# Performance work log

Hardware: AMD Instinct MI355X
Metric: run time of the kernel (lower is better)

Reference implementation:

```python
import jax, jax.numpy as jnp
import numpy as np

ROUTING_ROUNDS = 3
EPS = 1e-9

def squash(s, axis):
    # s * ||s||^2 / (1 + ||s||^2) / ||s||
    sn = jnp.sum(s * s, axis=axis, keepdims=True)
    return s * (sn / (1.0 + sn)) * jax.lax.rsqrt(sn + EPS)

def setup_inputs() -> dict:
    key = jax.random.key(0)
    k1, k2 = jax.random.split(key)
    B, N, D = 32, 2048, 32   # batch, input caps num, input caps dim
    C, V = 64, 32            # output caps num, output caps dim
    input_layer = jax.random.normal(k1, (B, N, D), dtype=jnp.float32)
    W = 0.1 * jax.random.normal(k2, (1, N, C, V, D), dtype=jnp.float32)
    return {"input_layer": input_layer, "W": W}

def reference(input_layer, W):
    # input_layer: [B, N, D]; W: [1, N, C, V, D]
    B, N, D = input_layer.shape
    Wn = W[0]  # [N, C, V, D]
    C, V = Wn.shape[1], Wn.shape[2]
    # caps_predicted (u_hat): [B, N, C, V]  (== tf matmul of W_tiled @ caps_output_tiled, squeezed)
    u_hat = jnp.einsum('bnd,ncvd->bncv', input_layer, Wn)
    b = jnp.zeros((B, N, C), dtype=input_layer.dtype)
    v = None
    for _ in range(ROUTING_ROUNDS):
        r = jax.nn.softmax(b, axis=2)                      # [B, N, C]
        s = jnp.einsum('bnc,bncv->bcv', r, u_hat)          # weighted_sum over input caps
        v = squash(s, axis=-1)                             # [B, C, V]
        # agreement = u_hat^T . v : [B, N, C]
        b = b + jnp.einsum('bncv,bcv->bnc', u_hat, v)
    # match original output shape [B, 1, caps_num, vec_len, 1]
    return v[:, None, :, :, None]
```

## Files before the change

kernel.cpp:

```cpp
#include <hip/hip_runtime.h>
#include <hip/hip_bf16.h>


#define B_ 32
#define N_ 2048
#define D_ 32
#define C_ 64
#define V_ 32

typedef __attribute__((ext_vector_type(4))) float f32x4;
typedef __attribute__((ext_vector_type(4))) int i32x4;
typedef __bf16 bf16x8 __attribute__((ext_vector_type(8)));

__device__ __forceinline__ unsigned f2bf1(float f) {
  unsigned u = __builtin_bit_cast(unsigned, f);
  return (u + 0x7FFFu + ((u >> 16) & 1u)) >> 16;
}
__device__ __forceinline__ float bf2f(unsigned h) {
  unsigned u = h << 16;
  return __builtin_bit_cast(float, u);
}

__global__ __launch_bounds__(256) void uhat_kernel(const float* __restrict__ x,
                                                   const float* __restrict__ W,
                                                   unsigned short* __restrict__ uh) {
  const int n = blockIdx.x;
  const int wave = threadIdx.x >> 6;
  const int l = threadIdx.x & 63;
  const int l16 = l & 15, kg = l >> 4;

  __shared__ unsigned short lds[4][32 * 68];
  unsigned short* wlds = lds[wave];

  bf16x8 a[2];
#pragma unroll
  for (int mt = 0; mt < 2; ++mt) {
    const float* xp = x + (((size_t)(mt * 16 + l16)) * N_ + n) * D_ + kg * 8;
    f32x4 x0 = *(const f32x4*)xp;
    f32x4 x1 = *(const f32x4*)(xp + 4);
    i32x4 af;
    af[0] = f2bf1(x0[0]) | (f2bf1(x0[1]) << 16);
    af[1] = f2bf1(x0[2]) | (f2bf1(x0[3]) << 16);
    af[2] = f2bf1(x1[0]) | (f2bf1(x1[1]) << 16);
    af[3] = f2bf1(x1[2]) | (f2bf1(x1[3]) << 16);
    a[mt] = __builtin_bit_cast(bf16x8, af);
  }
  const f32x4 zero = {0.f, 0.f, 0.f, 0.f};
  const int br_f = l >> 1, half = l & 1;

  for (int ph = 0; ph < 8; ++ph) {
#pragma unroll
    for (int pt4 = 0; pt4 < 4; ++pt4) {
      const int p = wave * 512 + ph * 64 + pt4 * 16 + l16;
      const float* wp = W + ((size_t)n * 2048 + p) * D_ + kg * 8;
      f32x4 w0 = *(const f32x4*)wp;
      f32x4 w1 = *(const f32x4*)(wp + 4);
      i32x4 bv;
      bv[0] = f2bf1(w0[0]) | (f2bf1(w0[1]) << 16);
      bv[1] = f2bf1(w0[2]) | (f2bf1(w0[3]) << 16);
      bv[2] = f2bf1(w1[0]) | (f2bf1(w1[1]) << 16);
      bv[3] = f2bf1(w1[2]) | (f2bf1(w1[3]) << 16);
      bf16x8 bfrag = __builtin_bit_cast(bf16x8, bv);
#pragma unroll
      for (int mt = 0; mt < 2; ++mt) {
        f32x4 acc = __builtin_amdgcn_mfma_f32_16x16x32_bf16(a[mt], bfrag, zero, 0, 0, 0);
#pragma unroll
        for (int j = 0; j < 4; ++j) {
          const int br = mt * 16 + kg * 4 + j;
          wlds[br * 68 + pt4 * 16 + l16] = (unsigned short)f2bf1(acc[j]);
        }
      }
    }
    asm volatile("s_waitcnt lgkmcnt(0)" ::: "memory");
    __builtin_amdgcn_sched_barrier(0);
    {
      const unsigned short* src = wlds + br_f * 68 + half * 32;
      unsigned short* dst = uh + ((size_t)n * 32 + br_f) * 2048 +
                            (size_t)(wave * 512 + ph * 64 + half * 32);
      i32x4 v0 = *(const i32x4*)(src + 0);
      i32x4 v1 = *(const i32x4*)(src + 8);
      i32x4 v2 = *(const i32x4*)(src + 16);
      i32x4 v3 = *(const i32x4*)(src + 24);
      *(i32x4*)(dst + 0) = v0;
      *(i32x4*)(dst + 8) = v1;
      *(i32x4*)(dst + 16) = v2;
      *(i32x4*)(dst + 24) = v3;
    }
    asm volatile("s_waitcnt lgkmcnt(0)" ::: "memory");
    __builtin_amdgcn_sched_barrier(0);
  }
}

template <int ROUND>
__global__ __launch_bounds__(256) void routing_kernel(const unsigned short* __restrict__ uh,
                                                      const float* __restrict__ vsum,
                                                      float* __restrict__ part) {
  const int b = blockIdx.x >> 5;
  const int chunk = blockIdx.x & 31;
  const int wave = threadIdx.x >> 6;
  const int l = threadIdx.x & 63;

  float vs[32];
  if (ROUND >= 2) {
    const f32x4* vp = (const f32x4*)(vsum + ((size_t)b * 64 + l) * 32);
#pragma unroll
    for (int i = 0; i < 8; ++i) {
      f32x4 t = vp[i];
      vs[4 * i] = t[0]; vs[4 * i + 1] = t[1]; vs[4 * i + 2] = t[2]; vs[4 * i + 3] = t[3];
    }
  }
  float sacc[32];
#pragma unroll
  for (int v = 0; v < 32; ++v) sacc[v] = 0.f;

  const int n0 = chunk * 64 + wave * 16;
  for (int ni = 0; ni < 16; ++ni) {
    const int n = n0 + ni;
    const i32x4* up = (const i32x4*)(uh + ((size_t)n * 32 + b) * 2048 + l * 32);
    i32x4 qs0 = up[0], qs1 = up[1], qs2 = up[2], qs3 = up[3];
    float u[32];
#pragma unroll
    for (int i = 0; i < 4; ++i) {
      unsigned v0 = (unsigned)qs0[i], v1 = (unsigned)qs1[i], v2 = (unsigned)qs2[i], v3 = (unsigned)qs3[i];
      u[0 + 2 * i] = bf2f(v0 & 0xffffu);  u[0 + 2 * i + 1] = bf2f(v0 >> 16);
      u[8 + 2 * i] = bf2f(v1 & 0xffffu);  u[8 + 2 * i + 1] = bf2f(v1 >> 16);
      u[16 + 2 * i] = bf2f(v2 & 0xffffu); u[16 + 2 * i + 1] = bf2f(v2 >> 16);
      u[24 + 2 * i] = bf2f(v3 & 0xffffu); u[24 + 2 * i + 1] = bf2f(v3 >> 16);
    }
    float r;
    if (ROUND >= 2) {
      float br = 0.f;
#pragma unroll
      for (int v = 0; v < 32; ++v) br = fmaf(u[v], vs[v], br);
      float m = br;
#pragma unroll
      for (int off = 32; off; off >>= 1) m = fmaxf(m, __shfl_xor(m, off, 64));
      float e = __expf(br - m);
      float den = e;
#pragma unroll
      for (int off = 32; off; off >>= 1) den += __shfl_xor(den, off, 64);
      r = e / den;
    } else {
      r = 1.0f / 64.0f;
    }
#pragma unroll
    for (int v = 0; v < 32; ++v) sacc[v] = fmaf(r, u[v], sacc[v]);
  }

  __shared__ float red[4][64][33];
#pragma unroll
  for (int v = 0; v < 32; ++v) red[wave][l][v] = sacc[v];
  __syncthreads();
  const int t = threadIdx.x;
  f32x4 o0, o1;
#pragma unroll
  for (int i = 0; i < 4; ++i) {
    const int e0 = t * 8 + i, e1 = t * 8 + 4 + i;
    o0[i] = red[0][e0 >> 5][e0 & 31] + red[1][e0 >> 5][e0 & 31] +
            red[2][e0 >> 5][e0 & 31] + red[3][e0 >> 5][e0 & 31];
    o1[i] = red[0][e1 >> 5][e1 & 31] + red[1][e1 >> 5][e1 & 31] +
            red[2][e1 >> 5][e1 & 31] + red[3][e1 >> 5][e1 & 31];
  }
  float* pp = part + ((size_t)blockIdx.x) * 2048 + t * 8;
  *(f32x4*)pp = o0;
  *(f32x4*)(pp + 4) = o1;
}

template <int ROUND>
__global__ __launch_bounds__(256) void squash_kernel(const float* __restrict__ part,
                                                     float* __restrict__ vsum,
                                                     float* __restrict__ out) {
  const int t = blockIdx.x * 256 + threadIdx.x;
  const int b = t >> 11;
  const int e = t & 2047;
  float sv = 0.f;
#pragma unroll
  for (int k = 0; k < 32; ++k) sv += part[((size_t)(b * 32 + k)) * 2048 + e];
  float sq = sv * sv;
#pragma unroll
  for (int off = 16; off; off >>= 1) sq += __shfl_xor(sq, off, 64);
  float scale = (sq / (1.f + sq)) * rsqrtf(sq + 1e-9f);
  float val = sv * scale;
  out[t] = val;
  if (ROUND == 1) vsum[t] = val;
  else if (ROUND == 2) vsum[t] += val;
}

extern "C" void kernel_launch(void* const* d_in, const int* in_sizes, int n_in,
                              void* d_out, int out_size, void* d_ws, size_t ws_size,
                              hipStream_t stream) {
  const float* x = (const float*)d_in[0];
  const float* W = (const float*)d_in[1];
  float* out = (float*)d_out;

  const size_t UH_BYTES = (size_t)B_ * N_ * C_ * V_ * 2;
  const size_t PART_BYTES = (size_t)B_ * 32 * 2048 * 4;
  const size_t VSUM_BYTES = (size_t)B_ * C_ * V_ * 4;
  if (ws_size < UH_BYTES + PART_BYTES + VSUM_BYTES) return;

  unsigned short* uh = (unsigned short*)d_ws;
  float* part = (float*)((char*)d_ws + UH_BYTES);
  float* vsum = (float*)((char*)d_ws + UH_BYTES + PART_BYTES);

  uhat_kernel<<<N_, 256, 0, stream>>>(x, W, uh);
  routing_kernel<1><<<B_ * 32, 256, 0, stream>>>(uh, vsum, part);
  squash_kernel<1><<<256, 256, 0, stream>>>(part, vsum, out);
  routing_kernel<2><<<B_ * 32, 256, 0, stream>>>(uh, vsum, part);
  squash_kernel<2><<<256, 256, 0, stream>>>(part, vsum, out);
  routing_kernel<3><<<B_ * 32, 256, 0, stream>>>(uh, vsum, part);
  squash_kernel<3><<<256, 256, 0, stream>>>(part, vsum, out);
}
```

Baseline: 332.4 us.

## Prefetch next W phase into registers and double-buffer LDS staging in uhat

The uhat kernel now loads the next phase's W values into registers before computing the current phase, so the global load latency overlaps the MFMA, conversion and store work. The per-wave LDS staging buffer is doubled and alternates by phase, which makes it safe to drop the trailing LDS wait at the end of each phase. This costs more registers and twice the LDS. The uhat kernel streams a large amount of W data, so hiding its latency could help, though the routing kernels still make up much of the total time.

```diff
diff --git a/kernel.cpp b/kernel.cpp
--- a/kernel.cpp
+++ b/kernel.cpp
@@ -29,8 +29,7 @@
   const int l = threadIdx.x & 63;
   const int l16 = l & 15, kg = l >> 4;
 
-  __shared__ unsigned short lds[4][32 * 68];
-  unsigned short* wlds = lds[wave];
+  __shared__ unsigned short lds[2][4][32 * 68];
 
   bf16x8 a[2];
 #pragma unroll
@@ -47,14 +46,32 @@
   }
   const f32x4 zero = {0.f, 0.f, 0.f, 0.f};
   const int br_f = l >> 1, half = l & 1;
-
+  const float* wbase = W + ((size_t)n * 2048 + wave * 512 + l16) * D_ + kg * 8;
+
+  f32x4 wreg[8];
+#pragma unroll
+  for (int pt4 = 0; pt4 < 4; ++pt4) {
+    const float* wp = wbase + (size_t)(pt4 * 16) * D_;
+    wreg[2 * pt4] = *(const f32x4*)wp;
+    wreg[2 * pt4 + 1] = *(const f32x4*)(wp + 4);
+  }
+
+#pragma unroll
   for (int ph = 0; ph < 8; ++ph) {
+    unsigned short* wlds = lds[ph & 1][wave];
+    f32x4 wnext[8];
+    if (ph < 7) {
+#pragma unroll
+      for (int pt4 = 0; pt4 < 4; ++pt4) {
+        const float* wp = wbase + (size_t)((ph + 1) * 64 + pt4 * 16) * D_;
+        wnext[2 * pt4] = *(const f32x4*)wp;
+        wnext[2 * pt4 + 1] = *(const f32x4*)(wp + 4);
+      }
+      __builtin_amdgcn_sched_barrier(0);
+    }
 #pragma unroll
     for (int pt4 = 0; pt4 < 4; ++pt4) {
-      const int p = wave * 512 + ph * 64 + pt4 * 16 + l16;
-      const float* wp = W + ((size_t)n * 2048 + p) * D_ + kg * 8;
-      f32x4 w0 = *(const f32x4*)wp;
-      f32x4 w1 = *(const f32x4*)(wp + 4);
+      f32x4 w0 = wreg[2 * pt4], w1 = wreg[2 * pt4 + 1];
       i32x4 bv;
       bv[0] = f2bf1(w0[0]) | (f2bf1(w0[1]) << 16);
       bv[1] = f2bf1(w0[2]) | (f2bf1(w0[3]) << 16);
@@ -86,8 +103,11 @@
       *(i32x4*)(dst + 16) = v2;
       *(i32x4*)(dst + 24) = v3;
     }
-    asm volatile("s_waitcnt lgkmcnt(0)" ::: "memory");
     __builtin_amdgcn_sched_barrier(0);
+    if (ph < 7) {
+#pragma unroll
+      for (int i = 0; i < 8; ++i) wreg[i] = wnext[i];
+    }
   }
 }
 
```

Result: no change. 330.7 us (-0.5%).
